# Kernel tuning notes

Measured on AMD Instinct MI355X. Metric: run time of the kernel, lower is better.

The kernel has to match this reference:

```python
import jax, jax.numpy as jnp
import numpy as np

EMBED = 768
HEADS = 12
B, S = 32, 1024


def setup_inputs() -> dict:
    key = jax.random.key(0)
    k1, k2, k3 = jax.random.split(key, 3)
    scale_in = 1.0 / np.sqrt(EMBED)
    x = jax.random.normal(k1, (B, S, EMBED), dtype=jnp.float32)
    # weights stored [in, out] (transpose of torch Linear layout)
    w_qkv = jax.random.normal(k2, (EMBED, 3 * EMBED), dtype=jnp.float32) * scale_in
    b_qkv = jnp.zeros((3 * EMBED,), dtype=jnp.float32)
    w_o = jax.random.normal(k3, (EMBED, EMBED), dtype=jnp.float32) * scale_in
    b_o = jnp.zeros((EMBED,), dtype=jnp.float32)
    return {"x": x, "w_qkv": w_qkv, "b_qkv": b_qkv, "w_o": w_o, "b_o": b_o}


def reference(x, w_qkv, b_qkv, w_o, b_o):
    Bt, St, E = x.shape
    H = HEADS
    Dh = E // H
    qkv = x @ w_qkv + b_qkv                      # [B, S, 3E]
    qkv = qkv.reshape(Bt, St, H, 3 * Dh)          # [B, S, H, 3Dh]
    q, k, v = jnp.split(qkv, 3, axis=-1)          # each [B, S, H, Dh]
    # NOTE: faithful to source — attention over the HEADS axis per token,
    # scaled by embed_size**-0.5 (not head_dim**-0.5).
    attn = jnp.einsum('bshd,bsgd->bshg', q, k) * (E ** -0.5)  # [B, S, H, H]
    attn = jax.nn.softmax(attn, axis=-1)
    out = jnp.einsum('bshg,bsgd->bshd', attn, v)  # [B, S, H, Dh]
    out = out.reshape(Bt, St, E)
    return out @ w_o + b_o
```

## Files before the change

### kernel.cpp

```cpp
#include <hip/hip_runtime.h>
#include <hip/hip_bf16.h>

#define EMBED 768
#define HEADS 12
#define TOKENS 32768
#define QKVN  (3*EMBED)
#define KDIM  768
#define QK_SCALE 0.03608439182435161f

typedef __attribute__((ext_vector_type(8))) __bf16 bf16x8;
typedef __attribute__((ext_vector_type(4))) __bf16 bf16x4;
typedef __attribute__((ext_vector_type(4))) float  f32x4;

__device__ __forceinline__ void gload_lds16(const void* gptr, void* lptr) {
    __builtin_amdgcn_global_load_lds(
        (const __attribute__((address_space(1))) void*)gptr,
        (__attribute__((address_space(3))) void*)lptr,
        16, 0, 0);
}

__global__ __launch_bounds__(256) void k_cvt_bf16(const float4* __restrict__ src,
                                                  bf16x4* __restrict__ dst, int n4) {
    int i = blockIdx.x * blockDim.x + threadIdx.x;
    int stride = gridDim.x * blockDim.x;
    for (; i < n4; i += stride) {
        float4 f = src[i];
        bf16x4 o;
        o[0] = (__bf16)f.x; o[1] = (__bf16)f.y; o[2] = (__bf16)f.z; o[3] = (__bf16)f.w;
        dst[i] = o;
    }
}

__global__ __launch_bounds__(256) void k_transpose_cvt(const float* __restrict__ src,
                                                       __bf16* __restrict__ dst,
                                                       int R, int C) {
    __shared__ float tile[32][33];
    int c0 = blockIdx.x * 32, r0 = blockIdx.y * 32;
    int tx = threadIdx.x, ty = threadIdx.y;
#pragma unroll
    for (int j = 0; j < 4; j++) {
        int r = r0 + ty + j * 8;
        tile[ty + j * 8][tx] = src[(long)r * C + c0 + tx];
    }
    __syncthreads();
#pragma unroll
    for (int j = 0; j < 4; j++) {
        int c = c0 + ty + j * 8;
        dst[(long)c * R + r0 + tx] = (__bf16)tile[tx][ty + j * 8];
    }
}

template <typename OutT>
__global__ __launch_bounds__(512, 2) void gemm8(const __bf16* __restrict__ A,
                                                const __bf16* __restrict__ Bt,
                                                const float* __restrict__ bias,
                                                OutT* __restrict__ C, int N) {
    extern __shared__ char lds[];
    const int tid = threadIdx.x;
    const int w = tid >> 6, lane = tid & 63;
    const int wr = w >> 2, wc = w & 3;
    const int l15 = lane & 15, l16 = lane >> 4;
    const int K = KDIM;

    const int nbx = N >> 8;
    const int nwg = gridDim.x;
    const int cpx = nwg >> 3;
    const int bid = blockIdx.x;
    const int swz = (bid & 7) * cpx + (bid >> 3);
    const int brow = swz / nbx, bcol = swz % nbx;
    const long arow0 = (long)brow * 256;
    const long ncol0 = (long)bcol * 256;

#define AOFF(b, mh) (((b) * 2 + (mh)) * 16384)
#define BOFF(b, kh) (65536 + ((b) * 2 + (kh)) * 16384)

    const int rA0 = tid >> 3;
    const int cbA = ((tid & 7) * 16) ^ ((rA0 & 7) << 4);
    const int rB0 = tid >> 2;
    const int kbB = (((tid & 3) ^ ((tid >> 3) & 3)) * 16);
    const int ldsw = w * 1024;

    auto stageA = [&](int b, int mh, int kt) {
#pragma unroll
        for (int j = 0; j < 2; ++j) {
            const __bf16* g = A + (arow0 + mh * 128 + j * 64 + rA0) * K + kt * 64 + (cbA >> 1);
            gload_lds16(g, lds + AOFF(b, mh) + j * 8192 + ldsw);
        }
    };
    auto stageB = [&](int b, int kh, int kt) {
#pragma unroll
        for (int j = 0; j < 2; ++j) {
            const __bf16* g = Bt + (ncol0 + j * 128 + rB0) * K + kt * 64 + kh * 32 + (kbB >> 1);
            gload_lds16(g, lds + BOFF(b, kh) + j * 8192 + ldsw);
        }
    };

    const int xorv = (lane & 7) << 4;
    const int arow_part = (wr * 16 + l15) * 128;
    const int aco0 = arow_part + ((l16 * 16) ^ xorv);
    const int aco1 = arow_part + ((64 + l16 * 16) ^ xorv);
    const int bco = (wc * 16 + l15) * 64 + ((l16 ^ ((l15 >> 1) & 3)) * 16);

    f32x4 acc[8][4] = {};

#define BLOAD(bb, kh) \
    _Pragma("unroll") for (int g = 0; g < 4; ++g) \
        bfr[g] = *(const bf16x8*)(lds + BOFF(bb, kh) + g * 4096 + bco);

#define PHASE(bb, mq, kh, BL, STAGE, WAIT) { \
    BL \
    _Pragma("unroll") for (int f = 0; f < 4; ++f) \
        af[f] = *(const bf16x8*)(lds + AOFF(bb, mq) + f * 4096 + ((kh) ? aco1 : aco0)); \
    STAGE; \
    __builtin_amdgcn_s_barrier(); \
    asm volatile("s_waitcnt lgkmcnt(0)" ::: "memory"); \
    __builtin_amdgcn_sched_barrier(0); \
    __builtin_amdgcn_s_setprio(1); \
    _Pragma("unroll") for (int f = 0; f < 4; ++f) \
        _Pragma("unroll") for (int g = 0; g < 4; ++g) \
            acc[(mq) * 4 + f][g] = __builtin_amdgcn_mfma_f32_16x16x32_bf16(af[f], bfr[g], acc[(mq) * 4 + f][g], 0, 0, 0); \
    __builtin_amdgcn_s_setprio(0); \
    WAIT; \
    __builtin_amdgcn_s_barrier(); \
    __builtin_amdgcn_sched_barrier(0); \
}

    stageA(0, 0, 0); stageB(0, 0, 0); stageA(0, 1, 0); stageB(0, 1, 0);
    stageB(1, 0, 1); stageA(1, 0, 1);
    asm volatile("s_waitcnt vmcnt(4)" ::: "memory");
    __builtin_amdgcn_s_barrier();
    __builtin_amdgcn_sched_barrier(0);

    for (int i = 0; i < 5; ++i) {
        const int t = 2 * i;
        bf16x8 af[4], bfr[4];
        PHASE(0, 0, 0, BLOAD(0, 0), stageB(1, 1, t + 1), );
        PHASE(0, 1, 0, ,            stageA(1, 1, t + 1), );
        PHASE(0, 0, 1, BLOAD(0, 1), stageB(0, 0, t + 2), );
        PHASE(0, 1, 1, ,            stageA(0, 0, t + 2), asm volatile("s_waitcnt vmcnt(4)" ::: "memory"));
        PHASE(1, 0, 0, BLOAD(1, 0), stageA(0, 1, t + 2), );
        PHASE(1, 1, 0, ,            stageB(0, 1, t + 2), );
        PHASE(1, 0, 1, BLOAD(1, 1), stageB(1, 0, t + 3), );
        PHASE(1, 1, 1, ,            stageA(1, 0, t + 3), asm volatile("s_waitcnt vmcnt(4)" ::: "memory"));
    }
    {
        bf16x8 af[4], bfr[4];
        PHASE(0, 0, 0, BLOAD(0, 0), stageB(1, 1, 11), );
        PHASE(0, 1, 0, ,            stageA(1, 1, 11), );
        PHASE(0, 0, 1, BLOAD(0, 1), , );
        PHASE(0, 1, 1, ,            , asm volatile("s_waitcnt vmcnt(0)" ::: "memory"));
        PHASE(1, 0, 0, BLOAD(1, 0), , );
        PHASE(1, 1, 0, ,            , );
        PHASE(1, 0, 1, BLOAD(1, 1), , );
        PHASE(1, 1, 1, ,            , );
    }
#undef PHASE
#undef BLOAD
#undef AOFF
#undef BOFF

#pragma unroll
    for (int mf = 0; mf < 8; ++mf) {
        const int row = (int)arow0 + mf * 32 + wr * 16 + l16 * 4;
#pragma unroll
        for (int g = 0; g < 4; ++g) {
            const int col = (int)ncol0 + g * 64 + wc * 16 + l15;
            const float bv = bias[col];
#pragma unroll
            for (int j = 0; j < 4; ++j) {
                C[(long)(row + j) * N + col] = (OutT)(acc[mf][g][j] + bv);
            }
        }
    }
}

#define HPITCH 200
__global__ __launch_bounds__(256) void k_attn(const __bf16* __restrict__ qkv,
                                              __bf16* __restrict__ out) {
    __shared__ __bf16 rows[4][12 * HPITCH];
    __shared__ float wts[4][144];
    const int w = threadIdx.x >> 6, lane = threadIdx.x & 63;
    const long token = (long)blockIdx.x * 4 + w;
    const __bf16* rp = qkv + token * QKVN;
    __bf16* row = rows[w];
    float* wt  = wts[w];

#pragma unroll
    for (int i = 0; i < 4; i++) {
        int c = i * 64 + lane;
        int h = c / 24;
        *(bf16x8*)(row + h * HPITCH + (c * 8 - h * 192)) = *(const bf16x8*)(rp + c * 8);
    }
    if (lane < 32) {
        int c = 256 + lane;
        int h = c / 24;
        *(bf16x8*)(row + h * HPITCH + (c * 8 - h * 192)) = *(const bf16x8*)(rp + c * 8);
    }
    __syncthreads();

    for (int p = lane; p < 144; p += 64) {
        int h = p / 12, g = p - h * 12;
        const __bf16* qp = row + h * HPITCH;
        const __bf16* kp = row + g * HPITCH + 64;
        float s = 0.f;
#pragma unroll
        for (int d = 0; d < 64; d += 8) {
            bf16x8 qv = *(const bf16x8*)(qp + d);
            bf16x8 kv = *(const bf16x8*)(kp + d);
#pragma unroll
            for (int j = 0; j < 8; j++) s += (float)qv[j] * (float)kv[j];
        }
        wt[p] = s * QK_SCALE;
    }
    __syncthreads();

    if (lane < 12) {
        float s[12];
#pragma unroll
        for (int g = 0; g < 12; g++) s[g] = wt[lane * 12 + g];
        float m = s[0];
#pragma unroll
        for (int g = 1; g < 12; g++) m = fmaxf(m, s[g]);
        float sum = 0.f;
#pragma unroll
        for (int g = 0; g < 12; g++) { s[g] = __expf(s[g] - m); sum += s[g]; }
        float inv = 1.0f / sum;
#pragma unroll
        for (int g = 0; g < 12; g++) wt[lane * 12 + g] = s[g] * inv;
    }
    __syncthreads();

    float vr[12];
#pragma unroll
    for (int g = 0; g < 12; g++) vr[g] = (float)row[g * HPITCH + 128 + lane];
#pragma unroll
    for (int h = 0; h < 12; h++) {
        float a = 0.f;
#pragma unroll
        for (int g = 0; g < 12; g++) a += wt[h * 12 + g] * vr[g];
        out[token * EMBED + h * 64 + lane] = (__bf16)a;
    }
}

extern "C" void kernel_launch(void* const* d_in, const int* in_sizes, int n_in,
                              void* d_out, int out_size, void* d_ws, size_t ws_size,
                              hipStream_t stream) {
    const float* x     = (const float*)d_in[0];
    const float* w_qkv = (const float*)d_in[1];
    const float* b_qkv = (const float*)d_in[2];
    const float* w_o   = (const float*)d_in[3];
    const float* b_o   = (const float*)d_in[4];
    float* out = (float*)d_out;

    char* ws = (char*)d_ws;
    size_t off = 0;
    auto take = [&](size_t bytes) {
        char* p = ws + off;
        off += (bytes + 255) & ~(size_t)255;
        return p;
    };
    __bf16* wqkvt = (__bf16*)take((size_t)QKVN * EMBED * 2);
    __bf16* wot   = (__bf16*)take((size_t)EMBED * EMBED * 2);
    __bf16* xb    = (__bf16*)take((size_t)TOKENS * EMBED * 2);
    __bf16* qkvb  = (__bf16*)take((size_t)TOKENS * QKVN * 2);
    __bf16* attno = xb;

    static bool attr_done = false;
    if (!attr_done) {
        hipFuncSetAttribute((const void*)gemm8<__bf16>,
                            hipFuncAttributeMaxDynamicSharedMemorySize, 131072);
        hipFuncSetAttribute((const void*)gemm8<float>,
                            hipFuncAttributeMaxDynamicSharedMemorySize, 131072);
        attr_done = true;
    }

    int n4 = TOKENS * EMBED / 4;
    k_cvt_bf16<<<2048, 256, 0, stream>>>((const float4*)x, (bf16x4*)xb, n4);

    dim3 tb(32, 8);
    k_transpose_cvt<<<dim3(QKVN / 32, EMBED / 32), tb, 0, stream>>>(w_qkv, wqkvt, EMBED, QKVN);
    k_transpose_cvt<<<dim3(EMBED / 32, EMBED / 32), tb, 0, stream>>>(w_o, wot, EMBED, EMBED);

    gemm8<__bf16><<<(TOKENS / 256) * (QKVN / 256), 512, 131072, stream>>>(
        xb, wqkvt, b_qkv, qkvb, QKVN);

    k_attn<<<TOKENS / 4, 256, 0, stream>>>(qkvb, attno);

    gemm8<float><<<(TOKENS / 256) * (EMBED / 256), 512, 131072, stream>>>(
        attno, wot, b_o, out, EMBED);
}
```

Before: 274.5 us.

## Double-buffer LDS fragment reads to overlap with MFMA in GEMM main loop

The GEMM main loop now reads the next phase's A/B fragments from LDS into a second register set while the current phase's MFMAs run. It waits only on partial lgkmcnt counts instead of draining to zero, and the global-to-LDS staging order and vmcnt waits are rescheduled to match. The goal is to hide LDS read latency behind matrix math. The cost is more VGPRs for the duplicated fragment buffers, and the hand-tuned wait counts are fragile to get right.

```diff
diff --git a/kernel.cpp b/kernel.cpp
--- a/kernel.cpp
+++ b/kernel.cpp
@@ -103,59 +103,67 @@
 
     f32x4 acc[8][4] = {};
 
-#define BLOAD(bb, kh) \
+#define RD_A(DST, BB, MQ, KH) do { \
+    _Pragma("unroll") for (int f = 0; f < 4; ++f) \
+        DST[f] = *(const bf16x8*)(lds + AOFF(BB, MQ) + f * 4096 + ((KH) ? aco1 : aco0)); \
+} while (0)
+#define RD_B(DST, BB, KH) do { \
     _Pragma("unroll") for (int g = 0; g < 4; ++g) \
-        bfr[g] = *(const bf16x8*)(lds + BOFF(bb, kh) + g * 4096 + bco);
-
-#define PHASE(bb, mq, kh, BL, STAGE, WAIT) { \
-    BL \
-    _Pragma("unroll") for (int f = 0; f < 4; ++f) \
-        af[f] = *(const bf16x8*)(lds + AOFF(bb, mq) + f * 4096 + ((kh) ? aco1 : aco0)); \
-    STAGE; \
+        DST[g] = *(const bf16x8*)(lds + BOFF(BB, KH) + g * 4096 + bco); \
+} while (0)
+#define VM6 asm volatile("s_waitcnt vmcnt(6)" ::: "memory")
+#define VM4 asm volatile("s_waitcnt vmcnt(4)" ::: "memory")
+#define VM2 asm volatile("s_waitcnt vmcnt(2)" ::: "memory")
+#define VM0 asm volatile("s_waitcnt vmcnt(0)" ::: "memory")
+
+#define PHASE(MQ, AF, BF, RD, ST, VW, LG) do { \
+    RD; ST; \
     __builtin_amdgcn_s_barrier(); \
-    asm volatile("s_waitcnt lgkmcnt(0)" ::: "memory"); \
+    asm volatile("s_waitcnt lgkmcnt(" LG ")" ::: "memory"); \
     __builtin_amdgcn_sched_barrier(0); \
     __builtin_amdgcn_s_setprio(1); \
     _Pragma("unroll") for (int f = 0; f < 4; ++f) \
         _Pragma("unroll") for (int g = 0; g < 4; ++g) \
-            acc[(mq) * 4 + f][g] = __builtin_amdgcn_mfma_f32_16x16x32_bf16(af[f], bfr[g], acc[(mq) * 4 + f][g], 0, 0, 0); \
+            acc[(MQ) * 4 + f][g] = __builtin_amdgcn_mfma_f32_16x16x32_bf16(AF[f], BF[g], acc[(MQ) * 4 + f][g], 0, 0, 0); \
     __builtin_amdgcn_s_setprio(0); \
-    WAIT; \
+    VW; \
     __builtin_amdgcn_s_barrier(); \
     __builtin_amdgcn_sched_barrier(0); \
-}
+} while (0)
 
     stageA(0, 0, 0); stageB(0, 0, 0); stageA(0, 1, 0); stageB(0, 1, 0);
-    stageB(1, 0, 1); stageA(1, 0, 1);
-    asm volatile("s_waitcnt vmcnt(4)" ::: "memory");
+    stageB(1, 0, 1); stageB(1, 1, 1); stageA(1, 0, 1); stageA(1, 1, 1);
+    VM6;
     __builtin_amdgcn_s_barrier();
     __builtin_amdgcn_sched_barrier(0);
+    bf16x8 afs0[4], afs1[4], bfs0[4], bfs1[4];
+    RD_A(afs0, 0, 0, 0); RD_B(bfs0, 0, 0);
+    asm volatile("s_waitcnt lgkmcnt(0)" ::: "memory");
+    __builtin_amdgcn_sched_barrier(0);
+    __builtin_amdgcn_s_barrier();
 
     for (int i = 0; i < 5; ++i) {
         const int t = 2 * i;
-        bf16x8 af[4], bfr[4];
-        PHASE(0, 0, 0, BLOAD(0, 0), stageB(1, 1, t + 1), );
-        PHASE(0, 1, 0, ,            stageA(1, 1, t + 1), );
-        PHASE(0, 0, 1, BLOAD(0, 1), stageB(0, 0, t + 2), );
-        PHASE(0, 1, 1, ,            stageA(0, 0, t + 2), asm volatile("s_waitcnt vmcnt(4)" ::: "memory"));
-        PHASE(1, 0, 0, BLOAD(1, 0), stageA(0, 1, t + 2), );
-        PHASE(1, 1, 0, ,            stageB(0, 1, t + 2), );
-        PHASE(1, 0, 1, BLOAD(1, 1), stageB(1, 0, t + 3), );
-        PHASE(1, 1, 1, ,            stageA(1, 0, t + 3), asm volatile("s_waitcnt vmcnt(4)" ::: "memory"));
-    }
-    {
-        bf16x8 af[4], bfr[4];
-        PHASE(0, 0, 0, BLOAD(0, 0), stageB(1, 1, 11), );
-        PHASE(0, 1, 0, ,            stageA(1, 1, 11), );
-        PHASE(0, 0, 1, BLOAD(0, 1), , );
-        PHASE(0, 1, 1, ,            , asm volatile("s_waitcnt vmcnt(0)" ::: "memory"));
-        PHASE(1, 0, 0, BLOAD(1, 0), , );
-        PHASE(1, 1, 0, ,            , );
-        PHASE(1, 0, 1, BLOAD(1, 1), , );
-        PHASE(1, 1, 1, ,            , );
-    }
+        PHASE(0, afs0, bfs0, RD_A(afs1, 0, 1, 0),                       ,                                    VM6, "4");
+        PHASE(1, afs1, bfs0, RD_A(afs0, 0, 0, 1); RD_B(bfs1, 0, 1),     stageB(0, 0, t + 2),                 VM6, "8");
+        PHASE(0, afs0, bfs1, RD_A(afs1, 0, 1, 1),                       ,                                    VM4, "4");
+        PHASE(1, afs1, bfs1, RD_A(afs0, 1, 0, 0); RD_B(bfs0, 1, 0),     stageA(0, 0, t + 2),                 VM4, "8");
+        PHASE(0, afs0, bfs0, RD_A(afs1, 1, 1, 0),                       stageB(0, 1, t + 2); stageA(0, 1, t + 2), VM6, "4");
+        PHASE(1, afs1, bfs0, RD_A(afs0, 1, 0, 1); RD_B(bfs1, 1, 1),     stageB(1, 0, t + 3),                 VM6, "8");
+        PHASE(0, afs0, bfs1, RD_A(afs1, 1, 1, 1),                       stageB(1, 1, t + 3),                 VM6, "4");
+        PHASE(1, afs1, bfs1, RD_A(afs0, 0, 0, 0); RD_B(bfs0, 0, 0),     stageA(1, 0, t + 3); stageA(1, 1, t + 3), VM6, "8");
+    }
+    PHASE(0, afs0, bfs0, RD_A(afs1, 0, 1, 0),                       , ,    "4");
+    PHASE(1, afs1, bfs0, RD_A(afs0, 0, 0, 1); RD_B(bfs1, 0, 1),     , ,    "8");
+    PHASE(0, afs0, bfs1, RD_A(afs1, 0, 1, 1),                       , VM2, "4");
+    PHASE(1, afs1, bfs1, RD_A(afs0, 1, 0, 0); RD_B(bfs0, 1, 0),     , VM0, "8");
+    PHASE(0, afs0, bfs0, RD_A(afs1, 1, 1, 0),                       , ,    "4");
+    PHASE(1, afs1, bfs0, RD_A(afs0, 1, 0, 1); RD_B(bfs1, 1, 1),     , ,    "8");
+    PHASE(0, afs0, bfs1, RD_A(afs1, 1, 1, 1),                       , ,    "4");
+    PHASE(1, afs1, bfs1, ,                                          , ,    "0");
 #undef PHASE
-#undef BLOAD
+#undef RD_A
+#undef RD_B
 #undef AOFF
 #undef BOFF
 
```

Result: no change. 272.7 us (-0.6%).

## Replace 256x256 GEMM with 128x256 tile, 4 waves, triple-buffered K=32 pipeline

Applied to the files above, without the earlier changes.

The GEMM kernel moves from a 512-thread block computing a 256x256 tile to a 256-thread block computing a 128x256 tile. Each wave now owns a 128x64 slice of the output. The K loop now takes K=32 steps through a three-stage LDS ring of 72 KB instead of the double-buffered 128 KB, which may allow more blocks per CU and shorten pipeline fill. The trade-off is lower operand reuse per block and more barriers per unit of K, since each step issues only 32 MFMAs per wave between syncs.

```diff
diff --git a/kernel.cpp b/kernel.cpp
--- a/kernel.cpp
+++ b/kernel.cpp
@@ -51,14 +51,14 @@
 }
 
 template <typename OutT>
-__global__ __launch_bounds__(512, 2) void gemm8(const __bf16* __restrict__ A,
-                                                const __bf16* __restrict__ Bt,
-                                                const float* __restrict__ bias,
-                                                OutT* __restrict__ C, int N) {
+__global__ __launch_bounds__(256, 2) void gemm_kt(const __bf16* __restrict__ A,
+                                                  const __bf16* __restrict__ Bt,
+                                                  const float* __restrict__ bias,
+                                                  OutT* __restrict__ C, int N) {
     extern __shared__ char lds[];
     const int tid = threadIdx.x;
     const int w = tid >> 6, lane = tid & 63;
-    const int wr = w >> 2, wc = w & 3;
+    const int wc = w;
     const int l15 = lane & 15, l16 = lane >> 4;
     const int K = KDIM;
 
@@ -68,107 +68,82 @@
     const int bid = blockIdx.x;
     const int swz = (bid & 7) * cpx + (bid >> 3);
     const int brow = swz / nbx, bcol = swz % nbx;
-    const long arow0 = (long)brow * 256;
+    const long arow0 = (long)brow * 128;
     const long ncol0 = (long)bcol * 256;
 
-#define AOFF(b, mh) (((b) * 2 + (mh)) * 16384)
-#define BOFF(b, kh) (65536 + ((b) * 2 + (kh)) * 16384)
-
-    const int rA0 = tid >> 3;
-    const int cbA = ((tid & 7) * 16) ^ ((rA0 & 7) << 4);
-    const int rB0 = tid >> 2;
-    const int kbB = (((tid & 3) ^ ((tid >> 3) & 3)) * 16);
-    const int ldsw = w * 1024;
-
-    auto stageA = [&](int b, int mh, int kt) {
-#pragma unroll
-        for (int j = 0; j < 2; ++j) {
-            const __bf16* g = A + (arow0 + mh * 128 + j * 64 + rA0) * K + kt * 64 + (cbA >> 1);
-            gload_lds16(g, lds + AOFF(b, mh) + j * 8192 + ldsw);
-        }
+    const int rowS = w * 16 + (lane >> 2);
+    const int cgS  = (((lane & 3) ^ ((lane >> 3) & 3)) * 8);
+    const int wofs = w * 1024;
+
+    auto stageA = [&](int r, int kt) {
+#pragma unroll
+        for (int j = 0; j < 2; ++j)
+            gload_lds16(A + (arow0 + j * 64 + rowS) * K + kt * 32 + cgS,
+                        lds + r * 8192 + j * 4096 + wofs);
     };
-    auto stageB = [&](int b, int kh, int kt) {
-#pragma unroll
-        for (int j = 0; j < 2; ++j) {
-            const __bf16* g = Bt + (ncol0 + j * 128 + rB0) * K + kt * 64 + kh * 32 + (kbB >> 1);
-            gload_lds16(g, lds + BOFF(b, kh) + j * 8192 + ldsw);
-        }
+    auto stageB = [&](int r, int kt) {
+#pragma unroll
+        for (int j = 0; j < 4; ++j)
+            gload_lds16(Bt + (ncol0 + j * 64 + rowS) * K + kt * 32 + cgS,
+                        lds + 24576 + r * 16384 + j * 4096 + wofs);
     };
 
-    const int xorv = (lane & 7) << 4;
-    const int arow_part = (wr * 16 + l15) * 128;
-    const int aco0 = arow_part + ((l16 * 16) ^ xorv);
-    const int aco1 = arow_part + ((64 + l16 * 16) ^ xorv);
-    const int bco = (wc * 16 + l15) * 64 + ((l16 ^ ((l15 >> 1) & 3)) * 16);
+    const int swz16 = (l16 ^ ((l15 >> 1) & 3)) * 16;
+    const int aco = l15 * 64 + swz16;
+    const int bco = wc * 4096 + l15 * 64 + swz16;
 
     f32x4 acc[8][4] = {};
 
-#define BLOAD(bb, kh) \
-    _Pragma("unroll") for (int g = 0; g < 4; ++g) \
-        bfr[g] = *(const bf16x8*)(lds + BOFF(bb, kh) + g * 4096 + bco);
-
-#define PHASE(bb, mq, kh, BL, STAGE, WAIT) { \
-    BL \
-    _Pragma("unroll") for (int f = 0; f < 4; ++f) \
-        af[f] = *(const bf16x8*)(lds + AOFF(bb, mq) + f * 4096 + ((kh) ? aco1 : aco0)); \
+#define VM6 asm volatile("s_waitcnt vmcnt(6)" ::: "memory")
+#define VM0 asm volatile("s_waitcnt vmcnt(0)" ::: "memory")
+#define KSTEP(R, STAGE, VW) do { \
+    bf16x8 af[8], bfv[4]; \
+    _Pragma("unroll") for (int mf = 0; mf < 8; ++mf) \
+        af[mf] = *(const bf16x8*)(lds + (R) * 8192 + mf * 1024 + aco); \
+    _Pragma("unroll") for (int n = 0; n < 4; ++n) \
+        bfv[n] = *(const bf16x8*)(lds + 24576 + (R) * 16384 + n * 1024 + bco); \
     STAGE; \
     __builtin_amdgcn_s_barrier(); \
     asm volatile("s_waitcnt lgkmcnt(0)" ::: "memory"); \
     __builtin_amdgcn_sched_barrier(0); \
     __builtin_amdgcn_s_setprio(1); \
-    _Pragma("unroll") for (int f = 0; f < 4; ++f) \
-        _Pragma("unroll") for (int g = 0; g < 4; ++g) \
-            acc[(mq) * 4 + f][g] = __builtin_amdgcn_mfma_f32_16x16x32_bf16(af[f], bfr[g], acc[(mq) * 4 + f][g], 0, 0, 0); \
+    _Pragma("unroll") for (int mf = 0; mf < 8; ++mf) \
+        _Pragma("unroll") for (int n = 0; n < 4; ++n) \
+            acc[mf][n] = __builtin_amdgcn_mfma_f32_16x16x32_bf16(af[mf], bfv[n], acc[mf][n], 0, 0, 0); \
     __builtin_amdgcn_s_setprio(0); \
-    WAIT; \
+    VW; \
     __builtin_amdgcn_s_barrier(); \
     __builtin_amdgcn_sched_barrier(0); \
-}
-
-    stageA(0, 0, 0); stageB(0, 0, 0); stageA(0, 1, 0); stageB(0, 1, 0);
-    stageB(1, 0, 1); stageA(1, 0, 1);
-    asm volatile("s_waitcnt vmcnt(4)" ::: "memory");
+} while (0)
+
+    stageA(0, 0); stageB(0, 0);
+    stageA(1, 1); stageB(1, 1);
+    VM6;
     __builtin_amdgcn_s_barrier();
     __builtin_amdgcn_sched_barrier(0);
 
-    for (int i = 0; i < 5; ++i) {
-        const int t = 2 * i;
-        bf16x8 af[4], bfr[4];
-        PHASE(0, 0, 0, BLOAD(0, 0), stageB(1, 1, t + 1), );
-        PHASE(0, 1, 0, ,            stageA(1, 1, t + 1), );
-        PHASE(0, 0, 1, BLOAD(0, 1), stageB(0, 0, t + 2), );
-        PHASE(0, 1, 1, ,            stageA(0, 0, t + 2), asm volatile("s_waitcnt vmcnt(4)" ::: "memory"));
-        PHASE(1, 0, 0, BLOAD(1, 0), stageA(0, 1, t + 2), );
-        PHASE(1, 1, 0, ,            stageB(0, 1, t + 2), );
-        PHASE(1, 0, 1, BLOAD(1, 1), stageB(1, 0, t + 3), );
-        PHASE(1, 1, 1, ,            stageA(1, 0, t + 3), asm volatile("s_waitcnt vmcnt(4)" ::: "memory"));
-    }
-    {
-        bf16x8 af[4], bfr[4];
-        PHASE(0, 0, 0, BLOAD(0, 0), stageB(1, 1, 11), );
-        PHASE(0, 1, 0, ,            stageA(1, 1, 11), );
-        PHASE(0, 0, 1, BLOAD(0, 1), , );
-        PHASE(0, 1, 1, ,            , asm volatile("s_waitcnt vmcnt(0)" ::: "memory"));
-        PHASE(1, 0, 0, BLOAD(1, 0), , );
-        PHASE(1, 1, 0, ,            , );
-        PHASE(1, 0, 1, BLOAD(1, 1), , );
-        PHASE(1, 1, 1, ,            , );
-    }
-#undef PHASE
-#undef BLOAD
-#undef AOFF
-#undef BOFF
+    for (int t = 0; t < 21; t += 3) {
+        KSTEP(0, stageA(2, t + 2); stageB(2, t + 2), VM6);
+        KSTEP(1, stageA(0, t + 3); stageB(0, t + 3), VM6);
+        KSTEP(2, stageA(1, t + 4); stageB(1, t + 4), VM6);
+    }
+    KSTEP(0, stageA(2, 23); stageB(2, 23), VM6);
+    KSTEP(1, , VM0);
+    KSTEP(2, , );
+#undef KSTEP
+#undef VM6
+#undef VM0
 
 #pragma unroll
     for (int mf = 0; mf < 8; ++mf) {
-        const int row = (int)arow0 + mf * 32 + wr * 16 + l16 * 4;
-#pragma unroll
-        for (int g = 0; g < 4; ++g) {
-            const int col = (int)ncol0 + g * 64 + wc * 16 + l15;
+        const int row = (int)arow0 + mf * 16 + l16 * 4;
+#pragma unroll
+        for (int n = 0; n < 4; ++n) {
+            const int col = (int)ncol0 + wc * 64 + n * 16 + l15;
             const float bv = bias[col];
 #pragma unroll
             for (int j = 0; j < 4; ++j) {
-                C[(long)(row + j) * N + col] = (OutT)(acc[mf][g][j] + bv);
+                C[(long)(row + j) * N + col] = (OutT)(acc[mf][n][j] + bv);
             }
         }
     }
@@ -267,9 +242,9 @@
 
     static bool attr_done = false;
     if (!attr_done) {
-        hipFuncSetAttribute((const void*)gemm8<__bf16>,
+        hipFuncSetAttribute((const void*)gemm_kt<__bf16>,
                             hipFuncAttributeMaxDynamicSharedMemorySize, 131072);
-        hipFuncSetAttribute((const void*)gemm8<float>,
+        hipFuncSetAttribute((const void*)gemm_kt<float>,
                             hipFuncAttributeMaxDynamicSharedMemorySize, 131072);
         attr_done = true;
     }
@@ -281,11 +256,11 @@
     k_transpose_cvt<<<dim3(QKVN / 32, EMBED / 32), tb, 0, stream>>>(w_qkv, wqkvt, EMBED, QKVN);
     k_transpose_cvt<<<dim3(EMBED / 32, EMBED / 32), tb, 0, stream>>>(w_o, wot, EMBED, EMBED);
 
-    gemm8<__bf16><<<(TOKENS / 256) * (QKVN / 256), 512, 131072, stream>>>(
+    gemm_kt<__bf16><<<(TOKENS / 128) * (QKVN / 256), 256, 73728, stream>>>(
         xb, wqkvt, b_qkv, qkvb, QKVN);
 
     k_attn<<<TOKENS / 4, 256, 0, stream>>>(qkvb, attno);
 
-    gemm8<float><<<(TOKENS / 256) * (EMBED / 256), 512, 131072, stream>>>(
+    gemm_kt<float><<<(TOKENS / 128) * (EMBED / 256), 256, 73728, stream>>>(
         attno, wot, b_o, out, EMBED);
 }
```

After: 253.9 us. -7.5%, faster.
